# Kernel optimization log

Measured on AMD Instinct MI355X. Metric: run time of the kernel, lower is better.

## Reference

```python
import jax, jax.numpy as jnp
import numpy as np

D = 1024      # embedding_dim
FW = 64       # filter_width
DEPTH = 2     # recurrence_depth
E = D * (DEPTH + 1)  # expanded dim = 3072
B, L = 2, 4096


def setup_inputs() -> dict:
    key = jax.random.key(0)
    ks = jax.random.split(key, 12)
    s = lambda k, shape, scale: jax.random.normal(k, shape, dtype=jnp.float32) * scale
    return {
        "x": jax.random.normal(ks[0], (B, L, D), dtype=jnp.float32),
        # input_projection: Linear(D, E)  (stored as [in,out])
        "w_in": s(ks[1], (D, E), 0.02), "b_in": jnp.zeros((E,), jnp.float32),
        # depthwise Conv1d(E, E, k=3, padding=2, groups=E): torch weight [E,1,3]
        "w_conv": s(ks[2], (E, 1, 3), 0.5), "b_conv": jnp.zeros((E,), jnp.float32),
        # HyenaFilter MLP: Linear(3,FW) -> SiLU -> Linear(FW,FW) -> SiLU -> Linear(FW, D, bias=False)
        "w1": s(ks[3], (3, FW), 0.5), "b1": jnp.zeros((FW,), jnp.float32),
        "w2": s(ks[4], (FW, FW), 0.1), "b2": jnp.zeros((FW,), jnp.float32),
        "w3": s(ks[5], (FW, D), 0.1),
        # HyenaFilter.bias parameter (output_channels = D*(DEPTH-1) = D)
        "filt_bias": jax.random.normal(ks[6], (D,), dtype=jnp.float32),
        # output_projection: Linear(D, D)
        "w_out": s(ks[7], (D, D), 0.02), "b_out": jnp.zeros((D,), jnp.float32),
    }


def _fftconv(x_bdl, h, bias_d):
    Lq = x_bdl.shape[-1]
    n = 2 * Lq
    Xf = jnp.fft.rfft(x_bdl, n=n)                       # [b,d,n//2+1]
    Hf = jnp.fft.rfft(h, n=n) / n                       # broadcast over [b,d]
    y = jnp.fft.irfft(Xf * Hf, n=n, norm="forward")[..., :Lq]
    return y + x_bdl * bias_d[:, None]


def reference(x, w_in, b_in, w_conv, b_conv, w1, b1, w2, b2, w3, filt_bias, w_out, b_out):
    _, Lx, Dm = x.shape
    # expand_input: Linear then b l e -> b e l
    u = (x @ w_in + b_in).transpose(0, 2, 1)            # [B,E,L]
    # depthwise short conv, padding=2 then truncate to L (causal-ish, as in source)
    u = jax.lax.conv_general_dilated(
        u, w_conv, window_strides=(1,), padding=[(2, 2)],
        feature_group_count=u.shape[1], dimension_numbers=("NCH", "OIH", "NCH"))
    u = (u + b_conv[None, :, None])[..., :Lx]
    streams = [u[:, i * Dm:(i + 1) * Dm, :] for i in range(DEPTH + 1)]  # each [B,D,L]
    # implicit filter generation
    t = jnp.linspace(0.0, 1.0, Lx)                       # [L]
    pos = jnp.tile(t[:, None], (1, 3))                   # [L,3]
    hmlp = jax.nn.silu(pos @ w1 + b1)
    hmlp = jax.nn.silu(hmlp @ w2 + b2)
    filters = (hmlp @ w3) * jnp.exp(-t[:, None] * jnp.abs(filt_bias)[None, :])  # [L,D]
    # recurrence (depth=2 -> single gated long conv); source indexes filters by ROW i
    v = streams[-1]
    for i in range(DEPTH - 1):
        v = v * streams[i]
        v = _fftconv(v, filters[i], filt_bias)
    # merge with stream 0, back to [B,L,D], output projection
    out = (v * streams[0]).transpose(0, 2, 1) @ w_out + b_out
    return out
```

## Files before the change

### kernel.cpp

```cpp
#include <hip/hip_runtime.h>
#include <hip/hip_bf16.h>


typedef __bf16 bf16x8 __attribute__((ext_vector_type(8)));
typedef float  f32x4  __attribute__((ext_vector_type(4)));

typedef const __attribute__((address_space(1))) unsigned int GU32;
typedef __attribute__((address_space(3))) unsigned int LU32;
#define GLL16(gp, lp) __builtin_amdgcn_global_load_lds((GU32*)(gp), (LU32*)(lp), 16, 0, 0)

#define CFENCE asm volatile("" ::: "memory")
#define SBAR   do { CFENCE; __builtin_amdgcn_s_barrier(); CFENCE; } while (0)
#define SCHEDB __builtin_amdgcn_sched_barrier(0)
#define VMCNT0 asm volatile("s_waitcnt vmcnt(0)" ::: "memory")

__device__ __forceinline__ float silu(float x) { return x / (1.f + __expf(-x)); }

__global__ __launch_bounds__(256) void hgen(const float* __restrict__ b1,
                                            const float* __restrict__ w2,
                                            const float* __restrict__ b2,
                                            const float* __restrict__ w3,
                                            float* __restrict__ h) {
    __shared__ float hm2[64];
    int t = threadIdx.x;
    if (t < 64) {
        float acc = b2[t];
        for (int f = 0; f < 64; ++f) acc += silu(b1[f]) * w2[f * 64 + t];
        hm2[t] = silu(acc);
    }
    __syncthreads();
    for (int r = 0; r < 4; ++r) {
        int j = t * 4 + r;
        float acc = 0.f;
        for (int g = 0; g < 64; ++g) acc += hm2[g] * w3[g * 1024 + j];
        h[j] = acc;
    }
}

__global__ void hfrag(const float* __restrict__ h, __bf16* __restrict__ af) {
    int sp = blockIdx.x;
    int lane = threadIdx.x;
    int m = lane & 15, kh = lane >> 4;
    bf16x8 v;
    #pragma unroll
    for (int j = 0; j < 8; ++j) {
        int k = kh * 8 + j;
        int idx = (k < 16) ? (32 * sp + m - k) : (32 * sp + 32 + m - k);
        float val = (idx >= 0 && idx < 1024) ? h[idx] : 0.f;
        v[j] = (__bf16)val;
    }
    *(bf16x8*)&af[(size_t)(sp * 64 + lane) * 8] = v;
}

__global__ __launch_bounds__(256) void cvt_x(const float* __restrict__ x,
                                             __bf16* __restrict__ xb) {
    size_t i = ((size_t)blockIdx.x * 256 + threadIdx.x) * 8;
    f32x4 a = *(const f32x4*)&x[i];
    f32x4 b = *(const f32x4*)&x[i + 4];
    bf16x8 v;
    v[0] = (__bf16)a[0]; v[1] = (__bf16)a[1]; v[2] = (__bf16)a[2]; v[3] = (__bf16)a[3];
    v[4] = (__bf16)b[0]; v[5] = (__bf16)b[1]; v[6] = (__bf16)b[2]; v[7] = (__bf16)b[3];
    *(bf16x8*)&xb[i] = v;
}

__global__ __launch_bounds__(256) void tcvt(const float* __restrict__ src,
                                            __bf16* __restrict__ dst,
                                            int ld, int cbase) {
    __shared__ __bf16 tile[64][65];
    int t = threadIdx.x;
    int k0 = blockIdx.x * 64, n0 = blockIdx.y * 64;
    int c = t & 63, rg = t >> 6;
    #pragma unroll
    for (int i = 0; i < 16; ++i) {
        int r = rg * 16 + i;
        tile[r][c] = (__bf16)src[(size_t)(k0 + r) * ld + cbase + n0 + c];
    }
    __syncthreads();
    #pragma unroll
    for (int i = 0; i < 16; ++i) {
        int nn = rg * 16 + i;
        dst[(size_t)(n0 + nn) * 1024 + k0 + c] = tile[c][nn];
    }
}

__device__ __forceinline__ void stage_half(const __bf16* __restrict__ panel, int kk,
                                           char* ldshalf, int t) {
    int c1 = t, c2 = t + 512;
    int s1 = c1 ^ (((c1 >> 5) & 1) << 1);
    int s2 = c2 ^ (((c2 >> 5) & 1) << 1);
    GLL16(panel + (size_t)(s1 >> 3) * 1024 + kk + (s1 & 7) * 8, ldshalf + c1 * 16);
    GLL16(panel + (size_t)(s2 >> 3) * 1024 + kk + (s2 & 7) * 8, ldshalf + c2 * 16);
}

__global__ __launch_bounds__(512, 1) void gemm256(const __bf16* __restrict__ A,
                                                  const __bf16* __restrict__ Bt,
                                                  const float* __restrict__ bias,
                                                  __bf16* __restrict__ out0,
                                                  __bf16* __restrict__ out1) {
    __shared__ __bf16 lds[65536];
    char* L = (char*)lds;
    int t = threadIdx.x, lane = t & 63, w = t >> 6;
    int wr = w >> 2, wc = w & 3;
    int m0 = blockIdx.x * 256, n0 = blockIdx.y * 256;
    int rl = lane & 15, kh8 = (lane >> 4) * 8;
    int nloc = (wc & 1) * 64;

    const __bf16* pa0 = A + (size_t)m0 * 1024;
    const __bf16* pa1 = A + (size_t)(m0 + 128) * 1024;
    const __bf16* pb0 = Bt + (size_t)n0 * 1024;
    const __bf16* pb1 = Bt + (size_t)(n0 + 128) * 1024;

    f32x4 acc[8][4] = {};
    bf16x8 ar[4][2], br[4][2];

#define RDA(dst, mf, ks) do { int _a = bA + ((mf) * 16 + rl) * 128 + ((ks) * 32 + kh8) * 2; \
        _a ^= ((_a >> 9) & 1) << 5; dst = *(const bf16x8*)(L + _a); } while (0)
#define RDB(dst, nf, ks) do { int _a = bB + (nloc + (nf) * 16 + rl) * 128 + ((ks) * 32 + kh8) * 2; \
        _a ^= ((_a >> 9) & 1) << 5; dst = *(const bf16x8*)(L + _a); } while (0)

    stage_half(pa0, 0, L, t);
    stage_half(pa1, 0, L + 16384, t);
    stage_half(pb0, 0, L + 65536, t);
    stage_half(pb1, 0, L + 65536 + 16384, t);
    VMCNT0;
    SBAR;

    for (int kt = 0; kt < 16; ++kt) {
        int p = kt & 1, q = p ^ 1;
        int bA = p * 32768 + wr * 16384;
        int bB = 65536 + p * 32768 + (wc >> 1) * 16384;
        int kk1 = (kt + 1) * 64;

        #pragma unroll
        for (int i = 0; i < 4; ++i) { RDA(ar[i][0], i, 0); RDA(ar[i][1], i, 1); }
        RDB(br[0][0], 0, 0); RDB(br[0][1], 0, 1);
        RDB(br[1][0], 1, 0); RDB(br[1][1], 1, 1);
        if (kt < 15) {
            stage_half(pa0, kk1, L + q * 32768, t);
            stage_half(pa1, kk1, L + q * 32768 + 16384, t);
        }
        SCHEDB; SBAR; SCHEDB;
        __builtin_amdgcn_s_setprio(1);
        #pragma unroll
        for (int mf = 0; mf < 4; ++mf)
            #pragma unroll
            for (int nf = 0; nf < 2; ++nf)
                #pragma unroll
                for (int ks = 0; ks < 2; ++ks)
                    acc[mf][nf] = __builtin_amdgcn_mfma_f32_16x16x32_bf16(ar[mf][ks], br[nf][ks], acc[mf][nf], 0, 0, 0);
        __builtin_amdgcn_s_setprio(0);
        SCHEDB; SBAR; SCHEDB;

        RDB(br[2][0], 2, 0); RDB(br[2][1], 2, 1);
        RDB(br[3][0], 3, 0); RDB(br[3][1], 3, 1);
        if (kt < 15) {
            stage_half(pb0, kk1, L + 65536 + q * 32768, t);
            stage_half(pb1, kk1, L + 65536 + q * 32768 + 16384, t);
        }
        SCHEDB; SBAR; SCHEDB;
        __builtin_amdgcn_s_setprio(1);
        #pragma unroll
        for (int mf = 0; mf < 4; ++mf)
            #pragma unroll
            for (int nf = 2; nf < 4; ++nf)
                #pragma unroll
                for (int ks = 0; ks < 2; ++ks)
                    acc[mf][nf] = __builtin_amdgcn_mfma_f32_16x16x32_bf16(ar[mf][ks], br[nf][ks], acc[mf][nf], 0, 0, 0);
        __builtin_amdgcn_s_setprio(0);
        SCHEDB; SBAR; SCHEDB;

        #pragma unroll
        for (int i = 0; i < 4; ++i) { RDA(ar[i][0], 4 + i, 0); RDA(ar[i][1], 4 + i, 1); }
        SCHEDB; SBAR; SCHEDB;
        __builtin_amdgcn_s_setprio(1);
        #pragma unroll
        for (int mf = 0; mf < 4; ++mf)
            #pragma unroll
            for (int nf = 0; nf < 2; ++nf)
                #pragma unroll
                for (int ks = 0; ks < 2; ++ks)
                    acc[4 + mf][nf] = __builtin_amdgcn_mfma_f32_16x16x32_bf16(ar[mf][ks], br[nf][ks], acc[4 + mf][nf], 0, 0, 0);
        __builtin_amdgcn_s_setprio(0);
        SCHEDB; SBAR; SCHEDB;

        __builtin_amdgcn_s_setprio(1);
        #pragma unroll
        for (int mf = 0; mf < 4; ++mf)
            #pragma unroll
            for (int nf = 2; nf < 4; ++nf)
                #pragma unroll
                for (int ks = 0; ks < 2; ++ks)
                    acc[4 + mf][nf] = __builtin_amdgcn_mfma_f32_16x16x32_bf16(ar[mf][ks], br[nf][ks], acc[4 + mf][nf], 0, 0, 0);
        __builtin_amdgcn_s_setprio(0);
        VMCNT0;
        SCHEDB; SBAR; SCHEDB;
    }
#undef RDA
#undef RDB

    int cb = lane & 15, rb = (lane >> 4) * 4;
    #pragma unroll
    for (int nf = 0; nf < 4; ++nf) {
        int col = n0 + wc * 64 + nf * 16 + cb;
        __bf16* uo = (col < 1024) ? out0 : out1;
        int oc = col & 1023;
        float bv = bias[(col < 1024) ? col : 1024 + col];
        #pragma unroll
        for (int mf = 0; mf < 8; ++mf) {
            int row = m0 + wr * 128 + mf * 16 + rb;
            #pragma unroll
            for (int j = 0; j < 4; ++j)
                uo[(size_t)(row + j) * 1024 + oc] = (__bf16)(acc[mf][nf][j] + bv);
        }
    }
}

template<int EPI>
__global__ __launch_bounds__(256) void gemm128(const __bf16* __restrict__ A,
                                               const __bf16* __restrict__ Bt,
                                               const float* __restrict__ bias,
                                               void* __restrict__ out0,
                                               void* __restrict__ out1) {
    __shared__ __bf16 As[128 * 32];
    __shared__ __bf16 Bs[128 * 32];
    int t = threadIdx.x, lane = t & 63, w = t >> 6;
    int m0 = blockIdx.x * 128, n0 = blockIdx.y * 128;
    int wr = (w >> 1) * 64, wc = (w & 1) * 64;
    f32x4 acc[4][4] = {};

    int s1 = w * 64 + lane;
    int s2 = s1 + 256;
    const __bf16* a1 = A + (size_t)(m0 + (s1 >> 2)) * 1024 + (s1 & 3) * 8;
    const __bf16* a2 = A + (size_t)(m0 + (s2 >> 2)) * 1024 + (s2 & 3) * 8;
    const __bf16* b1 = Bt + (size_t)(n0 + (s1 >> 2)) * 1024 + (s1 & 3) * 8;
    const __bf16* b2 = Bt + (size_t)(n0 + (s2 >> 2)) * 1024 + (s2 & 3) * 8;

    for (int kk = 0; kk < 1024; kk += 32) {
        GLL16(a1 + kk, (char*)&As[(size_t)s1 * 8]);
        GLL16(a2 + kk, (char*)&As[(size_t)s2 * 8]);
        GLL16(b1 + kk, (char*)&Bs[(size_t)s1 * 8]);
        GLL16(b2 + kk, (char*)&Bs[(size_t)s2 * 8]);
        __syncthreads();
        int kh = (lane >> 4) * 8, rl = lane & 15;
        bf16x8 af[4], bf[4];
        #pragma unroll
        for (int i = 0; i < 4; ++i) {
            af[i] = *(const bf16x8*)&As[(wr + i * 16 + rl) * 32 + kh];
            bf[i] = *(const bf16x8*)&Bs[(wc + i * 16 + rl) * 32 + kh];
        }
        #pragma unroll
        for (int mi = 0; mi < 4; ++mi)
            #pragma unroll
            for (int ni = 0; ni < 4; ++ni)
                acc[mi][ni] = __builtin_amdgcn_mfma_f32_16x16x32_bf16(af[mi], bf[ni], acc[mi][ni], 0, 0, 0);
        __syncthreads();
    }

    int cb = lane & 15, rb = (lane >> 4) * 4;
    #pragma unroll
    for (int ni = 0; ni < 4; ++ni) {
        int col = n0 + wc + ni * 16 + cb;
        if (EPI == 0) {
            __bf16* uo = (col < 1024) ? (__bf16*)out0 : (__bf16*)out1;
            int oc = col & 1023;
            float bv = bias[(col < 1024) ? col : 1024 + col];
            #pragma unroll
            for (int mi = 0; mi < 4; ++mi) {
                int row = m0 + wr + mi * 16 + rb;
                #pragma unroll
                for (int j = 0; j < 4; ++j)
                    uo[(size_t)(row + j) * 1024 + oc] = (__bf16)(acc[mi][ni][j] + bv);
            }
        } else {
            float* o = (float*)out0;
            float bv = bias[col];
            #pragma unroll
            for (int mi = 0; mi < 4; ++mi) {
                int row = m0 + wr + mi * 16 + rb;
                #pragma unroll
                for (int j = 0; j < 4; ++j)
                    o[(size_t)(row + j) * 1024 + col] = acc[mi][ni][j] + bv;
            }
        }
    }
}

__global__ __launch_bounds__(256) void convmul(const __bf16* __restrict__ u0,
                                               const __bf16* __restrict__ u2,
                                               const float* __restrict__ w_conv,
                                               const float* __restrict__ b_conv,
                                               __bf16* __restrict__ v,
                                               __bf16* __restrict__ st) {
    __shared__ float vt[64][65];
    int t = threadIdx.x;
    int b = blockIdx.z;
    int l0b = blockIdx.x * 64;
    int d0 = blockIdx.y * 64;
    int d = t & 63, lg = t >> 6;
    int col = d0 + d;
    int l0 = l0b + lg * 16;

    float c00 = w_conv[col * 3 + 0], c01 = w_conv[col * 3 + 1], c02 = w_conv[col * 3 + 2];
    float bc0 = b_conv[col];
    int e2 = 2048 + col;
    float c20 = w_conv[e2 * 3 + 0], c21 = w_conv[e2 * 3 + 1], c22 = w_conv[e2 * 3 + 2];
    float bc2 = b_conv[e2];

    size_t base = ((size_t)b * 4096 + l0) * 1024 + col;
    float p01 = (l0 >= 1) ? (float)u0[base - 1024] : 0.f;
    float p02 = (l0 >= 2) ? (float)u0[base - 2048] : 0.f;
    float p21 = (l0 >= 1) ? (float)u2[base - 1024] : 0.f;
    float p22 = (l0 >= 2) ? (float)u2[base - 2048] : 0.f;
    #pragma unroll
    for (int il = 0; il < 16; ++il) {
        float c0v = (float)u0[base + (size_t)il * 1024];
        float c2v = (float)u2[base + (size_t)il * 1024];
        float s0v = c00 * p02 + c01 * p01 + c02 * c0v + bc0;
        float s2v = c20 * p22 + c21 * p21 + c22 * c2v + bc2;
        p02 = p01; p01 = c0v; p22 = p21; p21 = c2v;
        vt[lg * 16 + il][d] = s0v * s2v;
        st[base + (size_t)il * 1024] = (__bf16)s0v;
    }
    __syncthreads();
    int lo = t & 63, dg = t >> 6;
    size_t obase = ((size_t)b * 1024 + d0 + dg * 16) * 4096 + l0b + lo;
    #pragma unroll
    for (int id = 0; id < 16; ++id)
        v[obase + (size_t)id * 4096] = (__bf16)vt[lo][dg * 16 + id];
}

__global__ __launch_bounds__(256) void firk(const __bf16* __restrict__ v,
                                            const __bf16* __restrict__ afg,
                                            const float* __restrict__ filt_bias,
                                            __bf16* __restrict__ z) {
    __shared__ __bf16 vlds[768 * 8];
    __shared__ __bf16 alds[33 * 64 * 8];
    int t = threadIdx.x;
    int bd = blockIdx.x;
    int d = bd & 1023;
    const __bf16* vrow = v + (size_t)bd * 4096;

    for (int c = t; c < 33 * 64; c += 256)
        *(bf16x8*)&alds[c * 8] = *(const bf16x8*)&afg[(size_t)c * 8];
    #pragma unroll
    for (int i = 0; i < 3; ++i) {
        int c = t + i * 256;
        bf16x8 val = {};
        if (c >= 130 && c < 642) val = *(const bf16x8*)&vrow[(c - 130) * 8];
        int cs = c ^ ((c >> 3) & 7);
        *(bf16x8*)&vlds[cs * 8] = val;
    }
    __syncthreads();

    int lane = t & 63, w = t >> 6;
    int n = lane & 15, kh = lane >> 4;
    int khoff = (kh == 0) ? 0 : (kh == 1) ? 8 : (kh == 2) ? -16 : -8;
    f32x4 acc[4] = {};
    for (int sp = 0; sp < 33; ++sp) {
        bf16x8 af = *(const bf16x8*)&alds[(sp * 64 + lane) * 8];
        #pragma unroll
        for (int ct = 0; ct < 4; ++ct) {
            int p = w * 64 + ct * 16 + n;
            int e = 16 * p - 32 * sp + 1040 + khoff;
            int c = e >> 3;
            int cs = c ^ ((c >> 3) & 7);
            bf16x8 bfv = *(const bf16x8*)&vlds[cs * 8];
            acc[ct] = __builtin_amdgcn_mfma_f32_16x16x32_bf16(af, bfv, acc[ct], 0, 0, 0);
        }
    }

    float fb = filt_bias[d];
    __bf16* zrow = z + (size_t)bd * 4096;
    #pragma unroll
    for (int ct = 0; ct < 4; ++ct) {
        int p = w * 64 + ct * 16 + n;
        #pragma unroll
        for (int j = 0; j < 4; ++j) {
            int l = 16 * p + kh * 4 + j;
            int e = l + 1040;
            int c = e >> 3;
            int cs = c ^ ((c >> 3) & 7);
            float vv = (float)vlds[cs * 8 + (e & 7)];
            zrow[l] = (__bf16)(acc[ct][j] + vv * fb);
        }
    }
}

__global__ __launch_bounds__(256) void trz(const __bf16* __restrict__ zz,
                                           const __bf16* __restrict__ st,
                                           __bf16* __restrict__ zt) {
    __shared__ __bf16 tile[64][65];
    int t = threadIdx.x;
    int l0 = blockIdx.x * 64, d0 = blockIdx.y * 64, b = blockIdx.z;
    int c = t & 63, rg = t >> 6;
    #pragma unroll
    for (int i = 0; i < 16; ++i) {
        int r = rg * 16 + i;
        tile[r][c] = zz[((size_t)(b * 1024 + d0 + r)) * 4096 + l0 + c];
    }
    __syncthreads();
    #pragma unroll
    for (int i = 0; i < 16; ++i) {
        int li = rg * 16 + i;
        size_t o = ((size_t)b * 4096 + l0 + li) * 1024 + d0 + c;
        zt[o] = (__bf16)((float)tile[c][li] * (float)st[o]);
    }
}

extern "C" void kernel_launch(void* const* d_in, const int* in_sizes, int n_in,
                              void* d_out, int out_size, void* d_ws, size_t ws_size,
                              hipStream_t stream) {
    const float* x      = (const float*)d_in[0];
    const float* w_in   = (const float*)d_in[1];
    const float* b_in   = (const float*)d_in[2];
    const float* w_conv = (const float*)d_in[3];
    const float* b_conv = (const float*)d_in[4];
    const float* b1     = (const float*)d_in[6];
    const float* w2     = (const float*)d_in[7];
    const float* b2     = (const float*)d_in[8];
    const float* w3     = (const float*)d_in[9];
    const float* fb     = (const float*)d_in[10];
    const float* w_out  = (const float*)d_in[11];
    const float* b_out  = (const float*)d_in[12];
    float* out = (float*)d_out;

    char* ws = (char*)d_ws;
    float*  h  = (float*)ws;
    __bf16* af = (__bf16*)(ws + 4096);
    const size_t SEG = (size_t)8192 * 1024;
    __bf16* X  = (__bf16*)(ws + 40960);
    __bf16* U0 = X + SEG;
    __bf16* U2 = U0 + SEG;
    __bf16* ST = U2 + SEG;
    __bf16* WT = ST + SEG - (size_t)2048 * 1024;

    hgen<<<1, 256, 0, stream>>>(b1, w2, b2, w3, h);
    hfrag<<<33, 64, 0, stream>>>(h, af);
    cvt_x<<<4096, 256, 0, stream>>>(x, X);
    tcvt<<<dim3(16, 16), 256, 0, stream>>>(w_in, WT, 3072, 0);
    tcvt<<<dim3(16, 16), 256, 0, stream>>>(w_in, WT + (size_t)1024 * 1024, 3072, 2048);
    gemm256<<<dim3(32, 8), 512, 0, stream>>>(X, WT, b_in, U0, U2);
    convmul<<<dim3(64, 16, 2), 256, 0, stream>>>(U0, U2, w_conv, b_conv, X, ST);
    firk<<<2048, 256, 0, stream>>>(X, af, fb, U2);
    tcvt<<<dim3(16, 16), 256, 0, stream>>>(w_out, X, 1024, 0);
    trz<<<dim3(64, 16, 2), 256, 0, stream>>>(U2, ST, U0);
    gemm128<1><<<dim3(64, 8), 256, 0, stream>>>(U0, X, b_out, (void*)out, nullptr);
}
```

Before: 268.3 us.

## Prefetch two k-tiles ahead in gemm256 and widen the LDS XOR swizzle

The GEMM prologue now loads two k-tiles into both LDS buffers, and the main loop issues loads for tile kt+2 into the buffer just consumed. It waits with vmcnt(8) so one stage of global loads stays in flight, which hides load latency better than the previous one-ahead scheme that drained to vmcnt(0) every iteration. The LDS swizzle changes from a single-bit XOR to a 3-bit XOR over the 16-byte chunks, meant to cut bank conflicts on the MFMA operand reads. This adds an extra barrier per iteration, and correctness depends on buffer reuse timing and the vmcnt accounting being exact.

```diff
diff --git a/kernel.cpp b/kernel.cpp
--- a/kernel.cpp
+++ b/kernel.cpp
@@ -12,6 +12,7 @@
 #define CFENCE asm volatile("" ::: "memory")
 #define SBAR   do { CFENCE; __builtin_amdgcn_s_barrier(); CFENCE; } while (0)
 #define SCHEDB __builtin_amdgcn_sched_barrier(0)
+#define VMCNT8 asm volatile("s_waitcnt vmcnt(8)" ::: "memory")
 #define VMCNT0 asm volatile("s_waitcnt vmcnt(0)" ::: "memory")
 
 __device__ __forceinline__ float silu(float x) { return x / (1.f + __expf(-x)); }
@@ -86,8 +87,8 @@
 __device__ __forceinline__ void stage_half(const __bf16* __restrict__ panel, int kk,
                                            char* ldshalf, int t) {
     int c1 = t, c2 = t + 512;
-    int s1 = c1 ^ (((c1 >> 5) & 1) << 1);
-    int s2 = c2 ^ (((c2 >> 5) & 1) << 1);
+    int s1 = c1 ^ ((c1 >> 3) & 7);
+    int s2 = c2 ^ ((c2 >> 3) & 7);
     GLL16(panel + (size_t)(s1 >> 3) * 1024 + kk + (s1 & 7) * 8, ldshalf + c1 * 16);
     GLL16(panel + (size_t)(s2 >> 3) * 1024 + kk + (s2 & 7) * 8, ldshalf + c2 * 16);
 }
@@ -114,31 +115,33 @@
     bf16x8 ar[4][2], br[4][2];
 
 #define RDA(dst, mf, ks) do { int _a = bA + ((mf) * 16 + rl) * 128 + ((ks) * 32 + kh8) * 2; \
-        _a ^= ((_a >> 9) & 1) << 5; dst = *(const bf16x8*)(L + _a); } while (0)
+        _a ^= (_a >> 3) & 0x70; dst = *(const bf16x8*)(L + _a); } while (0)
 #define RDB(dst, nf, ks) do { int _a = bB + (nloc + (nf) * 16 + rl) * 128 + ((ks) * 32 + kh8) * 2; \
-        _a ^= ((_a >> 9) & 1) << 5; dst = *(const bf16x8*)(L + _a); } while (0)
-
+        _a ^= (_a >> 3) & 0x70; dst = *(const bf16x8*)(L + _a); } while (0)
+
+    stage_half(pb0, 0, L + 65536, t);
+    stage_half(pb1, 0, L + 65536 + 16384, t);
     stage_half(pa0, 0, L, t);
     stage_half(pa1, 0, L + 16384, t);
-    stage_half(pb0, 0, L + 65536, t);
-    stage_half(pb1, 0, L + 65536 + 16384, t);
-    VMCNT0;
+    stage_half(pb0, 64, L + 65536 + 32768, t);
+    stage_half(pb1, 64, L + 65536 + 32768 + 16384, t);
+    stage_half(pa0, 64, L + 32768, t);
+    stage_half(pa1, 64, L + 32768 + 16384, t);
+    VMCNT8;
     SBAR;
 
     for (int kt = 0; kt < 16; ++kt) {
-        int p = kt & 1, q = p ^ 1;
+        int p = kt & 1;
         int bA = p * 32768 + wr * 16384;
         int bB = 65536 + p * 32768 + (wc >> 1) * 16384;
-        int kk1 = (kt + 1) * 64;
+        int kk2 = (kt + 2) * 64;
+        char* LA = L + p * 32768;
+        char* LB = L + 65536 + p * 32768;
 
         #pragma unroll
         for (int i = 0; i < 4; ++i) { RDA(ar[i][0], i, 0); RDA(ar[i][1], i, 1); }
         RDB(br[0][0], 0, 0); RDB(br[0][1], 0, 1);
         RDB(br[1][0], 1, 0); RDB(br[1][1], 1, 1);
-        if (kt < 15) {
-            stage_half(pa0, kk1, L + q * 32768, t);
-            stage_half(pa1, kk1, L + q * 32768 + 16384, t);
-        }
         SCHEDB; SBAR; SCHEDB;
         __builtin_amdgcn_s_setprio(1);
         #pragma unroll
@@ -153,10 +156,6 @@
 
         RDB(br[2][0], 2, 0); RDB(br[2][1], 2, 1);
         RDB(br[3][0], 3, 0); RDB(br[3][1], 3, 1);
-        if (kt < 15) {
-            stage_half(pb0, kk1, L + 65536 + q * 32768, t);
-            stage_half(pb1, kk1, L + 65536 + q * 32768 + 16384, t);
-        }
         SCHEDB; SBAR; SCHEDB;
         __builtin_amdgcn_s_setprio(1);
         #pragma unroll
@@ -171,6 +170,10 @@
 
         #pragma unroll
         for (int i = 0; i < 4; ++i) { RDA(ar[i][0], 4 + i, 0); RDA(ar[i][1], 4 + i, 1); }
+        if (kt < 14) {
+            stage_half(pb0, kk2, LB, t);
+            stage_half(pb1, kk2, LB + 16384, t);
+        }
         SCHEDB; SBAR; SCHEDB;
         __builtin_amdgcn_s_setprio(1);
         #pragma unroll
@@ -183,6 +186,11 @@
         __builtin_amdgcn_s_setprio(0);
         SCHEDB; SBAR; SCHEDB;
 
+        if (kt < 14) {
+            stage_half(pa0, kk2, LA, t);
+            stage_half(pa1, kk2, LA + 16384, t);
+        }
+        SCHEDB; SBAR; SCHEDB;
         __builtin_amdgcn_s_setprio(1);
         #pragma unroll
         for (int mf = 0; mf < 4; ++mf)
@@ -192,7 +200,8 @@
                 for (int ks = 0; ks < 2; ++ks)
                     acc[4 + mf][nf] = __builtin_amdgcn_mfma_f32_16x16x32_bf16(ar[mf][ks], br[nf][ks], acc[4 + mf][nf], 0, 0, 0);
         __builtin_amdgcn_s_setprio(0);
-        VMCNT0;
+        if (kt < 14)      { VMCNT8; }
+        else if (kt == 14){ VMCNT0; }
         SCHEDB; SBAR; SCHEDB;
     }
 #undef RDA
```

New measurement: 270.9 us. Within noise of the previous version (+0.9%).
